# Performance work log

Measured on AMD Instinct MI355X. Metric: run time of the kernel, lower is better.

Reference implementation:

```python
import jax, jax.numpy as jnp
import numpy as np

T = 2048   # block_size
V = 1024   # vocab_size
B = 8


def setup_inputs() -> dict:
    key = jax.random.key(0)
    k_idx, k_v = jax.random.split(key)
    idx = jax.random.randint(k_idx, (B, T), 0, V, dtype=jnp.int64 if jax.config.jax_enable_x64 else jnp.int32)
    # nn.Embedding(4,1) init: normal(mean=0, std=0.02) (the constant init is overwritten)
    v_weight = jax.random.normal(k_v, (4, 1), dtype=jnp.float32) * 0.02
    return {"idx": idx, "v_weight": v_weight}


def reference(idx, v_weight):
    # one-hot token 'embedding': [B, T, V]
    e = jax.nn.one_hot(idx, V, dtype=jnp.float32)

    # relative position table: pos[i,j] = i-j, clamped: <0 -> 3 (padding), >2 -> 2
    r = jnp.arange(T)
    d = r[:, None] - r[None, :]
    pidx = jnp.where(d < 0, 3, jnp.minimum(d, 2))            # [T, T] int

    tril = jnp.tril(jnp.ones((T, T), dtype=jnp.float32))     # lower-triangular mask

    # pos_embd = v(pos).squeeze().tril()
    pos_embd = v_weight[pidx, 0] * tril                      # [T, T]

    # layer_one = pos_embd @ e  -> [B, T, V]
    layer_one = jnp.einsum('ts,bsv->btv', pos_embd, e)

    # attention = e @ layer_one^T -> [B, T, T], then tril mask
    attention = jnp.einsum('btv,bsv->bts', e, layer_one)
    masked_attention = attention * tril                      # broadcast over batch

    # output = masked_attention @ e -> [B, T, V]
    logits = jnp.einsum('bts,bsv->btv', masked_attention, e)

    return jax.nn.softmax(logits, axis=-1)
```

## Files before the change

### kernel.cpp

```cpp
#include <hip/hip_runtime.h>

#define TT   2048
#define VV   1024
#define BB   8
#define NSEG 32
#define ROCC 32

#define SEGP_OFF 0
#define SEGH_OFF (1u << 20)
#define RANK_OFF (2u << 20)
#define OCC_OFF  ((2u << 20) + (1u << 16))

__global__ __launch_bounds__(64) void k_seghist(const int* __restrict__ idx,
                                                float* __restrict__ SEGH) {
    __shared__ float h[VV];
    const int bg = blockIdx.x, b = bg >> 5, g = bg & 31, lane = threadIdx.x;
    #pragma unroll
    for (int j = 0; j < 16; ++j) h[j * 64 + lane] = 0.0f;
    __syncthreads();
    const int x = idx[b * TT + (g << 6) + lane];
    atomicAdd(&h[x], 1.0f);
    __syncthreads();
    float* o = SEGH + (size_t)(b * NSEG + g) * VV;
    #pragma unroll
    for (int j = 0; j < 16; ++j) o[j * 64 + lane] = h[j * 64 + lane];
}

__global__ __launch_bounds__(256) void k_segprefix(const float* __restrict__ SEGH,
                                                   float* __restrict__ SEGP) {
    const int b = blockIdx.x, tid = threadIdx.x;
    float r0 = 0, r1 = 0, r2 = 0, r3 = 0;
    for (int g = 0; g < NSEG; ++g) {
        const size_t o = (size_t)(b * NSEG + g) * VV;
        SEGP[o + tid      ] = r0;  SEGP[o + tid + 256] = r1;
        SEGP[o + tid + 512] = r2;  SEGP[o + tid + 768] = r3;
        r0 += SEGH[o + tid      ];  r1 += SEGH[o + tid + 256];
        r2 += SEGH[o + tid + 512];  r3 += SEGH[o + tid + 768];
    }
}

__global__ __launch_bounds__(64) void k_rank(const int* __restrict__ idx,
                                             const float* __restrict__ SEGP,
                                             int* __restrict__ RANK,
                                             int* __restrict__ OCC) {
    const int bg = blockIdx.x, b = bg >> 5, g = bg & 31, lane = threadIdx.x;
    const int s = (g << 6) + lane;
    const int x = idx[b * TT + s];
    const int base = (int)SEGP[(size_t)(b * NSEG + g) * VV + x];
    int cnt = 0;
    for (int i = 0; i < 64; ++i) {
        const int xi = __shfl(x, i, 64);
        cnt += (i < lane && xi == x) ? 1 : 0;
    }
    const int rank = base + cnt + 1;
    RANK[b * TT + s] = rank;
    if (rank - 1 < ROCC) OCC[((size_t)b * VV + x) * ROCC + (rank - 1)] = s;
}

__global__ __launch_bounds__(256) void k_main(const int* __restrict__ idx,
                                              const float* __restrict__ w,
                                              const float* __restrict__ SEGP,
                                              const int* __restrict__ RANK,
                                              const int* __restrict__ OCC,
                                              float* __restrict__ out) {
    __shared__ float slab[4][VV];
    const int tid = threadIdx.x, lane = tid & 63, wid = tid >> 6;
    const int wg = blockIdx.x * 4 + wid;
    const int b = wg >> 11, t = wg & (TT - 1);

    const int* __restrict__ row = idx + b * TT;
    const int c = row[t];
    const int K = RANK[b * TT + t];
    const float w2 = w[2], dw0 = w[0] - w2, dw1 = w[1] - w2;
    const float Kf = (float)K;

    float* __restrict__ lg = slab[wid];
    #pragma unroll
    for (int j = 0; j < 16; ++j) lg[j * 64 + lane] = 0.0f;

    const float* __restrict__ segp_b = SEGP + (size_t)b * NSEG * VV;
    const int gt = t >> 6;

    float acc[16];
    {
        const float* __restrict__ pr = segp_b + (size_t)gt * VV;
        #pragma unroll
        for (int j = 0; j < 16; ++j) acc[j] = Kf * pr[j * 64 + lane];
    }
    if (lane <= (t & 63)) atomicAdd(&lg[row[(gt << 6) + lane]], Kf);

    const int* __restrict__ occ = OCC + ((size_t)b * VV + c) * ROCC;
    for (int j = 0; j < K; ++j) {
        const int p = occ[j] - 1;
        if (p >= 0) {
            const int gp = p >> 6;
            const float* __restrict__ pr = segp_b + (size_t)gp * VV;
            #pragma unroll
            for (int q = 0; q < 16; ++q) acc[q] -= pr[q * 64 + lane];
            if (lane <= (p & 63)) atomicAdd(&lg[row[(gp << 6) + lane]], -1.0f);
        }
    }

    asm volatile("s_waitcnt lgkmcnt(0)" ::: "memory");

    float lo[16];
    #pragma unroll
    for (int j = 0; j < 16; ++j) lo[j] = w2 * (acc[j] + lg[j * 64 + lane]);

    #pragma unroll
    for (int j = 0; j < 16; ++j)
        lo[j] += ((c >> 6) == j && (c & 63) == lane) ? dw0 * Kf : 0.0f;

    for (int j = 0; j < K - 1; ++j) {
        const int xn = row[occ[j] + 1];
        #pragma unroll
        for (int q = 0; q < 16; ++q)
            lo[q] += ((xn >> 6) == q && (xn & 63) == lane) ? dw1 : 0.0f;
    }

    float m = -1e30f;
    #pragma unroll
    for (int j = 0; j < 16; ++j) m = fmaxf(m, lo[j]);
    #pragma unroll
    for (int o = 32; o > 0; o >>= 1) m = fmaxf(m, __shfl_xor(m, o, 64));
    float sm = 0.0f;
    #pragma unroll
    for (int j = 0; j < 16; ++j) { lo[j] = __expf(lo[j] - m); sm += lo[j]; }
    #pragma unroll
    for (int o = 32; o > 0; o >>= 1) sm += __shfl_xor(sm, o, 64);
    const float inv = 1.0f / sm;

    float* __restrict__ op = out + ((size_t)wg << 10);
    #pragma unroll
    for (int j = 0; j < 16; ++j) op[j * 64 + lane] = lo[j] * inv;
}

extern "C" void kernel_launch(void* const* d_in, const int* in_sizes, int n_in,
                              void* d_out, int out_size, void* d_ws, size_t ws_size,
                              hipStream_t stream) {
    const int*   idx = (const int*)d_in[0];
    const float* w   = (const float*)d_in[1];
    float*       out = (float*)d_out;
    char* ws = (char*)d_ws;
    float* SEGP = (float*)(ws + SEGP_OFF);
    float* SEGH = (float*)(ws + SEGH_OFF);
    int*   RANK = (int*)(ws + RANK_OFF);
    int*   OCC  = (int*)(ws + OCC_OFF);

    k_seghist  <<<BB * NSEG, 64,  0, stream>>>(idx, SEGH);
    k_segprefix<<<BB,        256, 0, stream>>>(SEGH, SEGP);
    k_rank     <<<BB * NSEG, 64,  0, stream>>>(idx, SEGP, RANK, OCC);
    k_main     <<<(BB * TT) / 4, 256, 0, stream>>>(idx, w, SEGP, RANK, OCC, out);
}
```

Measured before the change: 102.9 us.

## Fuse setup kernels and compute rows per vocab symbol via incremental chains

```diff
diff --git a/kernel.cpp b/kernel.cpp
--- a/kernel.cpp
+++ b/kernel.cpp
@@ -3,136 +3,138 @@
 #define TT   2048
 #define VV   1024
 #define BB   8
-#define NSEG 32
 #define ROCC 32
 
 #define SEGP_OFF 0
-#define SEGH_OFF (1u << 20)
-#define RANK_OFF (2u << 20)
-#define OCC_OFF  ((2u << 20) + (1u << 16))
+#define TOT_OFF  (1u << 20)
+#define OCC_OFF  ((1u << 20) + (1u << 15))
 
-__global__ __launch_bounds__(64) void k_seghist(const int* __restrict__ idx,
-                                                float* __restrict__ SEGH) {
-    __shared__ float h[VV];
-    const int bg = blockIdx.x, b = bg >> 5, g = bg & 31, lane = threadIdx.x;
-    #pragma unroll
-    for (int j = 0; j < 16; ++j) h[j * 64 + lane] = 0.0f;
-    __syncthreads();
-    const int x = idx[b * TT + (g << 6) + lane];
-    atomicAdd(&h[x], 1.0f);
-    __syncthreads();
-    float* o = SEGH + (size_t)(b * NSEG + g) * VV;
-    #pragma unroll
-    for (int j = 0; j < 16; ++j) o[j * 64 + lane] = h[j * 64 + lane];
+__global__ __launch_bounds__(1024) void k_setup(const int* __restrict__ idx,
+                                                float* __restrict__ SEGP,
+                                                float* __restrict__ TOT,
+                                                int* __restrict__ OCC) {
+    __shared__ unsigned int hist[16][VV];
+    const int b = blockIdx.x, tid = threadIdx.x;
+    const int lane = tid & 63, w = tid >> 6;
+    const int* __restrict__ row = idx + b * TT;
+
+    unsigned run = 0;
+    for (int pass = 0; pass < 2; ++pass) {
+        #pragma unroll
+        for (int j = 0; j < 16; ++j) hist[j][tid] = 0u;
+        __syncthreads();
+
+        const int g   = pass * 16 + w;
+        const int s   = (g << 6) + lane;
+        const int tok = row[s];
+        atomicAdd(&hist[w][tok], 1u);
+        __syncthreads();
+
+        #pragma unroll
+        for (int j = 0; j < 16; ++j) {
+            const unsigned h = hist[j][tid];
+            hist[j][tid] = run;
+            SEGP[((size_t)b * 32 + pass * 16 + j) * VV + tid] = (float)run;
+            run += h;
+        }
+        __syncthreads();
+
+        int cnt = 0;
+        for (int i = 0; i < 64; ++i) {
+            const int xi = __shfl(tok, i, 64);
+            cnt += (i < lane && xi == tok) ? 1 : 0;
+        }
+        const int rank0 = (int)hist[w][tok] + cnt;
+        if (rank0 < ROCC) OCC[((size_t)b * VV + tok) * ROCC + rank0] = s;
+        __syncthreads();
+    }
+    TOT[b * VV + tid] = (float)run;
 }
 
-__global__ __launch_bounds__(256) void k_segprefix(const float* __restrict__ SEGH,
-                                                   float* __restrict__ SEGP) {
-    const int b = blockIdx.x, tid = threadIdx.x;
-    float r0 = 0, r1 = 0, r2 = 0, r3 = 0;
-    for (int g = 0; g < NSEG; ++g) {
-        const size_t o = (size_t)(b * NSEG + g) * VV;
-        SEGP[o + tid      ] = r0;  SEGP[o + tid + 256] = r1;
-        SEGP[o + tid + 512] = r2;  SEGP[o + tid + 768] = r3;
-        r0 += SEGH[o + tid      ];  r1 += SEGH[o + tid + 256];
-        r2 += SEGH[o + tid + 512];  r3 += SEGH[o + tid + 768];
-    }
-}
-
-__global__ __launch_bounds__(64) void k_rank(const int* __restrict__ idx,
-                                             const float* __restrict__ SEGP,
-                                             int* __restrict__ RANK,
-                                             int* __restrict__ OCC) {
-    const int bg = blockIdx.x, b = bg >> 5, g = bg & 31, lane = threadIdx.x;
-    const int s = (g << 6) + lane;
-    const int x = idx[b * TT + s];
-    const int base = (int)SEGP[(size_t)(b * NSEG + g) * VV + x];
-    int cnt = 0;
-    for (int i = 0; i < 64; ++i) {
-        const int xi = __shfl(x, i, 64);
-        cnt += (i < lane && xi == x) ? 1 : 0;
-    }
-    const int rank = base + cnt + 1;
-    RANK[b * TT + s] = rank;
-    if (rank - 1 < ROCC) OCC[((size_t)b * VV + x) * ROCC + (rank - 1)] = s;
-}
-
-__global__ __launch_bounds__(256) void k_main(const int* __restrict__ idx,
-                                              const float* __restrict__ w,
-                                              const float* __restrict__ SEGP,
-                                              const int* __restrict__ RANK,
-                                              const int* __restrict__ OCC,
-                                              float* __restrict__ out) {
+__global__ __launch_bounds__(256) void k_chain(const int* __restrict__ idx,
+                                               const float* __restrict__ wt,
+                                               const float* __restrict__ SEGP,
+                                               const float* __restrict__ TOT,
+                                               const int* __restrict__ OCC,
+                                               float* __restrict__ out) {
     __shared__ float slab[4][VV];
     const int tid = threadIdx.x, lane = tid & 63, wid = tid >> 6;
-    const int wg = blockIdx.x * 4 + wid;
-    const int b = wg >> 11, t = wg & (TT - 1);
+    const int gw = blockIdx.x * 4 + wid;
+    const int b = gw >> 10, c = gw & (VV - 1);
 
+    const int K0 = (int)TOT[b * VV + c];
+    if (K0 == 0) return;
+    const int K = (K0 < ROCC) ? K0 : ROCC;
+
+    const float w2 = wt[2], dw1 = wt[1] - w2;
+    const float wself = wt[0];
     const int* __restrict__ row = idx + b * TT;
-    const int c = row[t];
-    const int K = RANK[b * TT + t];
-    const float w2 = w[2], dw0 = w[0] - w2, dw1 = w[1] - w2;
-    const float Kf = (float)K;
+    const float* __restrict__ segp_b = SEGP + (size_t)b * 32 * VV;
+    const int* __restrict__ occ = OCC + ((size_t)b * VV + c) * ROCC;
 
     float* __restrict__ lg = slab[wid];
     #pragma unroll
-    for (int j = 0; j < 16; ++j) lg[j * 64 + lane] = 0.0f;
+    for (int q = 0; q < 16; ++q) lg[q * 64 + lane] = 0.0f;
 
-    const float* __restrict__ segp_b = SEGP + (size_t)b * NSEG * VV;
-    const int gt = t >> 6;
+    float A[16], Bg[16];
+    #pragma unroll
+    for (int q = 0; q < 16; ++q) { A[q] = 0.0f; Bg[q] = 0.0f; }
 
-    float acc[16];
-    {
-        const float* __restrict__ pr = segp_b + (size_t)gt * VV;
+    const int cq = c >> 6, cl = c & 63;
+
+    for (int j = 1; j <= K; ++j) {
+        const int u = occ[j - 1];
+        const int g = u >> 6, r = u & 63;
+
+        if (lane < r) atomicAdd(&lg[row[(g << 6) + lane]], 1.0f);
+
+        float D[16];
+        const float* __restrict__ pr = segp_b + (size_t)g * VV;
         #pragma unroll
-        for (int j = 0; j < 16; ++j) acc[j] = Kf * pr[j * 64 + lane];
-    }
-    if (lane <= (t & 63)) atomicAdd(&lg[row[(gt << 6) + lane]], Kf);
+        for (int q = 0; q < 16; ++q) D[q] = pr[q * 64 + lane];
 
-    const int* __restrict__ occ = OCC + ((size_t)b * VV + c) * ROCC;
-    for (int j = 0; j < K; ++j) {
-        const int p = occ[j] - 1;
-        if (p >= 0) {
-            const int gp = p >> 6;
-            const float* __restrict__ pr = segp_b + (size_t)gp * VV;
-            #pragma unroll
-            for (int q = 0; q < 16; ++q) acc[q] -= pr[q * 64 + lane];
-            if (lane <= (p & 63)) atomicAdd(&lg[row[(gp << 6) + lane]], -1.0f);
+        asm volatile("s_waitcnt lgkmcnt(0)" ::: "memory");
+        #pragma unroll
+        for (int q = 0; q < 16; ++q) {
+            D[q] += lg[q * 64 + lane];
+            lg[q * 64 + lane] = 0.0f;
         }
-    }
 
-    asm volatile("s_waitcnt lgkmcnt(0)" ::: "memory");
-
-    float lo[16];
-    #pragma unroll
-    for (int j = 0; j < 16; ++j) lo[j] = w2 * (acc[j] + lg[j * 64 + lane]);
-
-    #pragma unroll
-    for (int j = 0; j < 16; ++j)
-        lo[j] += ((c >> 6) == j && (c & 63) == lane) ? dw0 * Kf : 0.0f;
-
-    for (int j = 0; j < K - 1; ++j) {
-        const int xn = row[occ[j] + 1];
+        const float jf = (float)j;
+        float lo[16];
         #pragma unroll
         for (int q = 0; q < 16; ++q)
-            lo[q] += ((xn >> 6) == q && (xn & 63) == lane) ? dw1 : 0.0f;
+            lo[q] = w2 * (jf * D[q] - (A[q] + D[q])) + dw1 * Bg[q];
+        #pragma unroll
+        for (int q = 0; q < 16; ++q)
+            lo[q] += (q == cq && lane == cl) ? wself * jf : 0.0f;
+
+        #pragma unroll
+        for (int q = 0; q < 16; ++q) A[q] += D[q];
+        if (j < K && u + 1 < TT) {
+            const int xn = row[u + 1];
+            const int xq = xn >> 6, xl = xn & 63;
+            #pragma unroll
+            for (int q = 0; q < 16; ++q)
+                Bg[q] += (q == xq && lane == xl) ? 1.0f : 0.0f;
+        }
+
+        float m = -1e30f;
+        #pragma unroll
+        for (int q = 0; q < 16; ++q) m = fmaxf(m, lo[q]);
+        #pragma unroll
+        for (int o = 32; o > 0; o >>= 1) m = fmaxf(m, __shfl_xor(m, o, 64));
+        float sm = 0.0f;
+        #pragma unroll
+        for (int q = 0; q < 16; ++q) { lo[q] = __expf(lo[q] - m); sm += lo[q]; }
+        #pragma unroll
+        for (int o = 32; o > 0; o >>= 1) sm += __shfl_xor(sm, o, 64);
+        const float inv = 1.0f / sm;
+
+        float* __restrict__ op = out + ((size_t)(b * TT + u) << 10);
+        #pragma unroll
+        for (int q = 0; q < 16; ++q) op[q * 64 + lane] = lo[q] * inv;
     }
-
-    float m = -1e30f;
-    #pragma unroll
-    for (int j = 0; j < 16; ++j) m = fmaxf(m, lo[j]);
-    #pragma unroll
-    for (int o = 32; o > 0; o >>= 1) m = fmaxf(m, __shfl_xor(m, o, 64));
-    float sm = 0.0f;
-    #pragma unroll
-    for (int j = 0; j < 16; ++j) { lo[j] = __expf(lo[j] - m); sm += lo[j]; }
-    #pragma unroll
-    for (int o = 32; o > 0; o >>= 1) sm += __shfl_xor(sm, o, 64);
-    const float inv = 1.0f / sm;
-
-    float* __restrict__ op = out + ((size_t)wg << 10);
-    #pragma unroll
-    for (int j = 0; j < 16; ++j) op[j * 64 + lane] = lo[j] * inv;
 }
 
 extern "C" void kernel_launch(void* const* d_in, const int* in_sizes, int n_in,
@@ -143,12 +145,9 @@
     float*       out = (float*)d_out;
     char* ws = (char*)d_ws;
     float* SEGP = (float*)(ws + SEGP_OFF);
-    float* SEGH = (float*)(ws + SEGH_OFF);
-    int*   RANK = (int*)(ws + RANK_OFF);
+    float* TOT  = (float*)(ws + TOT_OFF);
     int*   OCC  = (int*)(ws + OCC_OFF);
 
-    k_seghist  <<<BB * NSEG, 64,  0, stream>>>(idx, SEGH);
-    k_segprefix<<<BB,        256, 0, stream>>>(SEGH, SEGP);
-    k_rank     <<<BB * NSEG, 64,  0, stream>>>(idx, SEGP, RANK, OCC);
-    k_main     <<<(BB * TT) / 4, 256, 0, stream>>>(idx, w, SEGP, RANK, OCC, out);
+    k_setup<<<BB, 1024, 0, stream>>>(idx, SEGP, TOT, OCC);
+    k_chain<<<(BB * VV) / 4, 256, 0, stream>>>(idx, w, SEGP, TOT, OCC, out);
 }
```

After: 103.6 us. No clear change (+0.7%).

## Use nearest segment-boundary prefix, single-wave blocks, capped occurrence loop, nontemporal stores

Applied to the files above, without the earlier changes.

```diff
diff --git a/kernel.cpp b/kernel.cpp
--- a/kernel.cpp
+++ b/kernel.cpp
@@ -6,37 +6,35 @@
 #define NSEG 32
 #define ROCC 32
 
-#define SEGP_OFF 0
-#define SEGH_OFF (1u << 20)
-#define RANK_OFF (2u << 20)
-#define OCC_OFF  ((2u << 20) + (1u << 16))
+#define SEGP_OFF 0x000000
+#define SEGH_OFF 0x110000
+#define RANK_OFF 0x210000
+#define OCC_OFF  0x220000
 
-__global__ __launch_bounds__(64) void k_seghist(const int* __restrict__ idx,
-                                                float* __restrict__ SEGH) {
-    __shared__ float h[VV];
+__global__ __launch_bounds__(64) void k_hist(const int* __restrict__ idx,
+                                             float* __restrict__ SEGH) {
+    __shared__ unsigned h[VV];
     const int bg = blockIdx.x, b = bg >> 5, g = bg & 31, lane = threadIdx.x;
     #pragma unroll
-    for (int j = 0; j < 16; ++j) h[j * 64 + lane] = 0.0f;
-    __syncthreads();
-    const int x = idx[b * TT + (g << 6) + lane];
-    atomicAdd(&h[x], 1.0f);
-    __syncthreads();
-    float* o = SEGH + (size_t)(b * NSEG + g) * VV;
+    for (int q = 0; q < 16; ++q) h[q * 64 + lane] = 0u;
+    asm volatile("s_waitcnt lgkmcnt(0)" ::: "memory");
+    const int tok = idx[b * TT + (g << 6) + lane];
+    atomicAdd(&h[tok], 1u);
+    asm volatile("s_waitcnt lgkmcnt(0)" ::: "memory");
+    float* __restrict__ o = SEGH + (size_t)(b * NSEG + g) * VV;
     #pragma unroll
-    for (int j = 0; j < 16; ++j) o[j * 64 + lane] = h[j * 64 + lane];
+    for (int q = 0; q < 16; ++q) o[q * 64 + lane] = (float)h[q * 64 + lane];
 }
 
-__global__ __launch_bounds__(256) void k_segprefix(const float* __restrict__ SEGH,
-                                                   float* __restrict__ SEGP) {
-    const int b = blockIdx.x, tid = threadIdx.x;
-    float r0 = 0, r1 = 0, r2 = 0, r3 = 0;
-    for (int g = 0; g < NSEG; ++g) {
-        const size_t o = (size_t)(b * NSEG + g) * VV;
-        SEGP[o + tid      ] = r0;  SEGP[o + tid + 256] = r1;
-        SEGP[o + tid + 512] = r2;  SEGP[o + tid + 768] = r3;
-        r0 += SEGH[o + tid      ];  r1 += SEGH[o + tid + 256];
-        r2 += SEGH[o + tid + 512];  r3 += SEGH[o + tid + 768];
-    }
+__global__ __launch_bounds__(1024) void k_prefix(const float* __restrict__ SEGH,
+                                                 float* __restrict__ SEGP) {
+    const int b = blockIdx.x, v = threadIdx.x;
+    const float* __restrict__ src = SEGH + (size_t)b * NSEG * VV + v;
+    float* __restrict__ dst = SEGP + (size_t)b * 33 * VV + v;
+    float run = 0.0f;
+    #pragma unroll
+    for (int g = 0; g < NSEG; ++g) { dst[g * VV] = run; run += src[g * VV]; }
+    dst[NSEG * VV] = run;
 }
 
 __global__ __launch_bounds__(64) void k_rank(const int* __restrict__ idx,
@@ -45,94 +43,102 @@
                                              int* __restrict__ OCC) {
     const int bg = blockIdx.x, b = bg >> 5, g = bg & 31, lane = threadIdx.x;
     const int s = (g << 6) + lane;
-    const int x = idx[b * TT + s];
-    const int base = (int)SEGP[(size_t)(b * NSEG + g) * VV + x];
+    const int tok = idx[b * TT + s];
+    const int base = (int)SEGP[(size_t)b * 33 * VV + (size_t)g * VV + tok];
     int cnt = 0;
     for (int i = 0; i < 64; ++i) {
-        const int xi = __shfl(x, i, 64);
-        cnt += (i < lane && xi == x) ? 1 : 0;
+        const int xi = __shfl(tok, i, 64);
+        cnt += (i < lane && xi == tok) ? 1 : 0;
     }
-    const int rank = base + cnt + 1;
-    RANK[b * TT + s] = rank;
-    if (rank - 1 < ROCC) OCC[((size_t)b * VV + x) * ROCC + (rank - 1)] = s;
+    const int r0 = base + cnt;
+    RANK[b * TT + s] = r0 + 1;
+    if (r0 < ROCC) OCC[((size_t)b * VV + tok) * ROCC + r0] = s;
 }
 
-__global__ __launch_bounds__(256) void k_main(const int* __restrict__ idx,
-                                              const float* __restrict__ w,
-                                              const float* __restrict__ SEGP,
-                                              const int* __restrict__ RANK,
-                                              const int* __restrict__ OCC,
-                                              float* __restrict__ out) {
-    __shared__ float slab[4][VV];
-    const int tid = threadIdx.x, lane = tid & 63, wid = tid >> 6;
-    const int wg = blockIdx.x * 4 + wid;
+__global__ __launch_bounds__(64) void k_main(const int* __restrict__ idx,
+                                             const float* __restrict__ wt,
+                                             const float* __restrict__ SEGP,
+                                             const int* __restrict__ RANK,
+                                             const int* __restrict__ OCC,
+                                             float* __restrict__ out) {
+    __shared__ float slab[VV];
+    const int lane = threadIdx.x;
+    const int wg = blockIdx.x;
     const int b = wg >> 11, t = wg & (TT - 1);
 
     const int* __restrict__ row = idx + b * TT;
     const int c = row[t];
     const int K = RANK[b * TT + t];
-    const float w2 = w[2], dw0 = w[0] - w2, dw1 = w[1] - w2;
+    const float w2 = wt[2], dw0 = wt[0] - w2, dw1 = wt[1] - w2;
     const float Kf = (float)K;
+    const float* __restrict__ segp_b = SEGP + (size_t)b * 33 * VV;
+    const int* __restrict__ occ = OCC + ((size_t)b * VV + c) * ROCC;
 
-    float* __restrict__ lg = slab[wid];
     #pragma unroll
-    for (int j = 0; j < 16; ++j) lg[j * 64 + lane] = 0.0f;
-
-    const float* __restrict__ segp_b = SEGP + (size_t)b * NSEG * VV;
-    const int gt = t >> 6;
+    for (int q = 0; q < 16; ++q) slab[q * 64 + lane] = 0.0f;
+    asm volatile("s_waitcnt lgkmcnt(0)" ::: "memory");
 
     float acc[16];
     {
-        const float* __restrict__ pr = segp_b + (size_t)gt * VV;
+        const int g = t >> 6, r = t & 63;
+        const int gd = (r < 32) ? g : g + 1;
+        const float* __restrict__ pr = segp_b + (size_t)gd * VV;
         #pragma unroll
-        for (int j = 0; j < 16; ++j) acc[j] = Kf * pr[j * 64 + lane];
+        for (int q = 0; q < 16; ++q) acc[q] = Kf * pr[q * 64 + lane];
+        const int tok = row[(g << 6) + lane];
+        if (r < 32) { if (lane <= r) atomicAdd(&slab[tok],  Kf); }
+        else        { if (lane >  r) atomicAdd(&slab[tok], -Kf); }
     }
-    if (lane <= (t & 63)) atomicAdd(&lg[row[(gt << 6) + lane]], Kf);
 
-    const int* __restrict__ occ = OCC + ((size_t)b * VV + c) * ROCC;
-    for (int j = 0; j < K; ++j) {
+    const int KK = (K < ROCC) ? K : ROCC;
+    for (int j = 0; j < KK; ++j) {
         const int p = occ[j] - 1;
-        if (p >= 0) {
-            const int gp = p >> 6;
-            const float* __restrict__ pr = segp_b + (size_t)gp * VV;
-            #pragma unroll
-            for (int q = 0; q < 16; ++q) acc[q] -= pr[q * 64 + lane];
-            if (lane <= (p & 63)) atomicAdd(&lg[row[(gp << 6) + lane]], -1.0f);
-        }
+        if (p < 0) continue;
+        const int g = p >> 6, r = p & 63;
+        const int gd = (r < 32) ? g : g + 1;
+        const float* __restrict__ pr = segp_b + (size_t)gd * VV;
+        #pragma unroll
+        for (int q = 0; q < 16; ++q) acc[q] -= pr[q * 64 + lane];
+        const int tok = row[(g << 6) + lane];
+        if (r < 32) { if (lane <= r) atomicAdd(&slab[tok], -1.0f); }
+        else        { if (lane >  r) atomicAdd(&slab[tok],  1.0f); }
     }
 
     asm volatile("s_waitcnt lgkmcnt(0)" ::: "memory");
+    #pragma unroll
+    for (int q = 0; q < 16; ++q)
+        acc[q] = w2 * (acc[q] + slab[q * 64 + lane]);
 
-    float lo[16];
-    #pragma unroll
-    for (int j = 0; j < 16; ++j) lo[j] = w2 * (acc[j] + lg[j * 64 + lane]);
-
-    #pragma unroll
-    for (int j = 0; j < 16; ++j)
-        lo[j] += ((c >> 6) == j && (c & 63) == lane) ? dw0 * Kf : 0.0f;
-
-    for (int j = 0; j < K - 1; ++j) {
-        const int xn = row[occ[j] + 1];
+    {
+        const int cq = c >> 6, cl = c & 63;
         #pragma unroll
         for (int q = 0; q < 16; ++q)
-            lo[q] += ((xn >> 6) == q && (xn & 63) == lane) ? dw1 : 0.0f;
+            acc[q] += (q == cq && lane == cl) ? dw0 * Kf : 0.0f;
+    }
+    for (int j = 0; j < KK - 1; ++j) {
+        const int xn = row[occ[j] + 1];
+        const int xq = xn >> 6, xl = xn & 63;
+        #pragma unroll
+        for (int q = 0; q < 16; ++q)
+            acc[q] += (q == xq && lane == xl) ? dw1 : 0.0f;
     }
 
     float m = -1e30f;
     #pragma unroll
-    for (int j = 0; j < 16; ++j) m = fmaxf(m, lo[j]);
+    for (int q = 0; q < 16; ++q) m = fmaxf(m, acc[q]);
     #pragma unroll
     for (int o = 32; o > 0; o >>= 1) m = fmaxf(m, __shfl_xor(m, o, 64));
     float sm = 0.0f;
     #pragma unroll
-    for (int j = 0; j < 16; ++j) { lo[j] = __expf(lo[j] - m); sm += lo[j]; }
+    for (int q = 0; q < 16; ++q) { acc[q] = __expf(acc[q] - m); sm += acc[q]; }
     #pragma unroll
     for (int o = 32; o > 0; o >>= 1) sm += __shfl_xor(sm, o, 64);
     const float inv = 1.0f / sm;
 
     float* __restrict__ op = out + ((size_t)wg << 10);
     #pragma unroll
-    for (int j = 0; j < 16; ++j) op[j * 64 + lane] = lo[j] * inv;
+    for (int q = 0; q < 16; ++q)
+        __builtin_nontemporal_store(acc[q] * inv, &op[q * 64 + lane]);
 }
 
 extern "C" void kernel_launch(void* const* d_in, const int* in_sizes, int n_in,
@@ -147,8 +153,8 @@
     int*   RANK = (int*)(ws + RANK_OFF);
     int*   OCC  = (int*)(ws + OCC_OFF);
 
-    k_seghist  <<<BB * NSEG, 64,  0, stream>>>(idx, SEGH);
-    k_segprefix<<<BB,        256, 0, stream>>>(SEGH, SEGP);
-    k_rank     <<<BB * NSEG, 64,  0, stream>>>(idx, SEGP, RANK, OCC);
-    k_main     <<<(BB * TT) / 4, 256, 0, stream>>>(idx, w, SEGP, RANK, OCC, out);
+    k_hist  <<<BB * NSEG, 64,   0, stream>>>(idx, SEGH);
+    k_prefix<<<BB,        1024, 0, stream>>>(SEGH, SEGP);
+    k_rank  <<<BB * NSEG, 64,   0, stream>>>(idx, SEGP, RANK, OCC);
+    k_main  <<<BB * TT,   64,   0, stream>>>(idx, w, SEGP, RANK, OCC, out);
 }
```

Result: faster. 94.28 us (-8.4%).
